# Kernel tuning notes

Hardware: AMD Instinct MI355X
Metric: run time of the kernel (lower is better)

The kernel has to match this reference:

```python
import jax, jax.numpy as jnp
import numpy as np

H = 1024
IN = 512
B = 32
E_H = 0.5
Z_MIN = 0.001
Z_MAX = 0.1
DT = 1.0


def setup_inputs() -> dict:
    key = jax.random.key(0)
    ks = jax.random.split(key, 10)
    s = 1.0 / np.sqrt(H)
    uni = lambda k, shape: jax.random.uniform(k, shape, jnp.float32, -s, s)
    return {
        "x": jax.random.normal(ks[0], (IN, B), jnp.float32),
        "h": jax.random.uniform(ks[1], (B, H), jnp.float32),      # hidden state [B,H]
        "X": jnp.ones((B, H, H), jnp.float32),                     # resources
        "U": jnp.full((B, H, H), 0.9, jnp.float32),                # utilization (init 0.9)
        "c_x": uni(ks[2], (H, H)),
        "c_u": uni(ks[3], (H, H)),
        "c_U": uni(ks[4], (H, H)),
        "c_h": uni(ks[5], (H, 1)),
        "w": uni(ks[6], (H, H)),
        "p": uni(ks[7], (H, IN)),
        "b": uni(ks[8], (H, 1)),
    }


def reference(x, h, X, U, c_x, c_u, c_U, c_h, w, p, b):
    sig = jax.nn.sigmoid
    hb = h[:, :, None]                                  # h[b,j] broadcast over k -> [B,H,1]
    # resource (X) update: z_x + (1-z_x)*X - dt*U*X*h
    z_x = Z_MIN + (Z_MAX - Z_MIN) * sig(c_x)            # [H,H]
    X_new = z_x + (1.0 - z_x) * X - DT * U * (X * hb)   # [B,H,H]
    # utilization (U) update, clamped to [Ucap (detached), 1]
    z_u = Z_MIN + (Z_MAX - Z_MIN) * sig(c_u)            # [H,H]
    Ucap = 0.9 * sig(c_U)                               # [H,H]
    U_new = Ucap * z_u + (1.0 - z_u) * U + DT * Ucap * ((1.0 - U) * hb)
    U_new = jnp.clip(U_new, jax.lax.stop_gradient(Ucap), 1.0)
    # hidden update with dynamic weights W = w * U * X (per batch)
    z_h = E_H * sig(c_h)                                # [H,1]
    W = w * U_new * X_new                               # [B,H,H]
    rec = jnp.einsum("bjk,bk->jb", W, h)               # [H,B]
    pre = rec + p @ x + b                               # [H,B]
    h_newT = (1.0 - z_h) * h.T + z_h * sig(pre)         # [H,B]
    return h_newT.T                                     # [B,H]
```

## Files before the change

### kernel.cpp

```cpp
#include <hip/hip_runtime.h>

#define HH 1024
#define INW 512
#define BB 32
#define BG 4
#define Z_MIN_C 0.001f
#define Z_RANGE_C 0.099f
#define E_H_C 0.5f

typedef float v4f __attribute__((ext_vector_type(4)));

__device__ __forceinline__ float sigmoidf_(float v) {
    return 1.0f / (1.0f + __expf(-v));
}

__global__ __launch_bounds__(256, 4) void stp_fused(
    const float* __restrict__ x,
    const float* __restrict__ h,
    const float* __restrict__ X,
    const float* __restrict__ U,
    const float* __restrict__ c_x,
    const float* __restrict__ c_u,
    const float* __restrict__ c_U,
    const float* __restrict__ c_h,
    const float* __restrict__ w,
    const float* __restrict__ p,
    const float* __restrict__ bias,
    float* __restrict__ out)
{
    const int j = blockIdx.x & (HH - 1);
    const int g = blockIdx.x >> 10;
    const int t = threadIdx.x;
    const int lane = t & 63;
    const int wave = t >> 6;
    const int k0 = t * 4;

    __shared__ float px_part[64][BG];
    __shared__ float rec_part[BG][4];

    v4f Xb[BG], Ub[BG], hkb[BG];
    float hjb[BG];
    #pragma unroll
    for (int i = 0; i < BG; ++i) {
        const int b = g * BG + i;
        const int rb = (b * HH + j) * HH + k0;
        Xb[i] = __builtin_nontemporal_load((const v4f*)(X + rb));
        Ub[i] = __builtin_nontemporal_load((const v4f*)(U + rb));
        hkb[i] = *(const v4f*)(h + b * HH + k0);
        hjb[i] = h[b * HH + j];
    }

    {
        const int b_id = t & 3;
        const int seg = t >> 2;
        const int b = g * BG + b_id;
        float acc = 0.0f;
        const float* prow = p + j * INW + seg * 8;
        const float* xcol = x + (seg * 8) * BB + b;
        #pragma unroll
        for (int i = 0; i < 8; ++i)
            acc = fmaf(prow[i], xcol[i * BB], acc);
        px_part[seg][b_id] = acc;
    }

    v4f cx4 = *(const v4f*)(c_x + j * HH + k0);
    v4f cu4 = *(const v4f*)(c_u + j * HH + k0);
    v4f cC4 = *(const v4f*)(c_U + j * HH + k0);
    v4f wv4 = *(const v4f*)(w + j * HH + k0);

    float zx[4], ozx[4], Acoef[4], ozu[4], Ucap[4], wr[4];
    #pragma unroll
    for (int c = 0; c < 4; ++c) {
        float zxx = Z_MIN_C + Z_RANGE_C * sigmoidf_(cx4[c]);
        float zuu = Z_MIN_C + Z_RANGE_C * sigmoidf_(cu4[c]);
        float ucc = 0.9f * sigmoidf_(cC4[c]);
        zx[c] = zxx;
        ozx[c] = 1.0f - zxx;
        ozu[c] = 1.0f - zuu;
        Ucap[c] = ucc;
        Acoef[c] = ucc * zuu;
        wr[c] = wv4[c];
    }

    float s[BG];
    #pragma unroll
    for (int i = 0; i < BG; ++i) {
        const float hjv = hjb[i];
        float ss = 0.0f;
        #pragma unroll
        for (int c = 0; c < 4; ++c) {
            float Xn = fmaf(ozx[c], Xb[i][c], zx[c]);
            Xn = fmaf(-Ub[i][c], Xb[i][c] * hjv, Xn);
            float Un = fmaf(ozu[c], Ub[i][c], Acoef[c]);
            Un = fmaf(Ucap[c] * hjv, 1.0f - Ub[i][c], Un);
            Un = fminf(fmaxf(Un, Ucap[c]), 1.0f);
            ss = fmaf(wr[c] * hkb[i][c], Un * Xn, ss);
        }
        s[i] = ss;
    }

    #pragma unroll
    for (int i = 0; i < BG; ++i) {
        float v = s[i];
        #pragma unroll
        for (int off = 32; off > 0; off >>= 1)
            v += __shfl_xor(v, off);
        if (lane == 0) rec_part[i][wave] = v;
    }
    __syncthreads();

    if (t < BG) {
        const int b = g * BG + t;
        float rec = rec_part[t][0] + rec_part[t][1] + rec_part[t][2] + rec_part[t][3];
        float px = 0.0f;
        #pragma unroll
        for (int sgi = 0; sgi < 64; ++sgi) px += px_part[sgi][t];
        float pre = rec + px + bias[j];
        float zh = E_H_C * sigmoidf_(c_h[j]);
        float hv = h[b * HH + j];
        out[b * HH + j] = (1.0f - zh) * hv + zh * sigmoidf_(pre);
    }
}

extern "C" void kernel_launch(void* const* d_in, const int* in_sizes, int n_in,
                              void* d_out, int out_size, void* d_ws, size_t ws_size,
                              hipStream_t stream) {
    const float* x   = (const float*)d_in[0];
    const float* h   = (const float*)d_in[1];
    const float* X   = (const float*)d_in[2];
    const float* U   = (const float*)d_in[3];
    const float* c_x = (const float*)d_in[4];
    const float* c_u = (const float*)d_in[5];
    const float* c_U = (const float*)d_in[6];
    const float* c_h = (const float*)d_in[7];
    const float* w   = (const float*)d_in[8];
    const float* p   = (const float*)d_in[9];
    const float* b   = (const float*)d_in[10];
    float* out = (float*)d_out;

    stp_fused<<<HH * 8, 256, 0, stream>>>(x, h, X, U, c_x, c_u, c_U, c_h, w, p, b, out);
}
```

Baseline: 299.8 us.

## Hoist p@x input projection into a separate precompute kernel

Moves the p@x + bias computation out of the fused kernel into a small prepass kernel that writes pre-activations to workspace. Before, each of the 8 batch-group blocks per row recomputed its own slice of p@x, so every p row was read 8 times, and the blocks needed shared-memory partials and a 64-term serial reduction. The main kernel now just reads one precomputed value per output. In exchange it adds a second launch and a workspace round trip. The prepass also reads x with a strided access pattern.

```diff
diff --git a/kernel.cpp b/kernel.cpp
--- a/kernel.cpp
+++ b/kernel.cpp
@@ -14,8 +14,30 @@
     return 1.0f / (1.0f + __expf(-v));
 }
 
+__global__ __launch_bounds__(256) void px_kernel(
+    const float* __restrict__ x,
+    const float* __restrict__ p,
+    const float* __restrict__ bias,
+    float* __restrict__ pre0)
+{
+    const int wv = threadIdx.x >> 6;
+    const int lane = threadIdx.x & 63;
+    const int j = blockIdx.x * 4 + wv;
+    const int b = lane & 31;
+    const int half = lane >> 5;
+
+    const float* pr = p + j * INW + half * 256;
+    const float* xc = x + (half * 256) * BB + b;
+    float acc = 0.0f;
+    #pragma unroll 8
+    for (int i = 0; i < 256; ++i)
+        acc = fmaf(pr[i], xc[i * BB], acc);
+    acc += __shfl_xor(acc, 32);
+    if (lane < 32)
+        pre0[lane * HH + j] = acc + bias[j];
+}
+
 __global__ __launch_bounds__(256, 4) void stp_fused(
-    const float* __restrict__ x,
     const float* __restrict__ h,
     const float* __restrict__ X,
     const float* __restrict__ U,
@@ -24,8 +46,7 @@
     const float* __restrict__ c_U,
     const float* __restrict__ c_h,
     const float* __restrict__ w,
-    const float* __restrict__ p,
-    const float* __restrict__ bias,
+    const float* __restrict__ pre0,
     float* __restrict__ out)
 {
     const int j = blockIdx.x & (HH - 1);
@@ -35,7 +56,6 @@
     const int wave = t >> 6;
     const int k0 = t * 4;
 
-    __shared__ float px_part[64][BG];
     __shared__ float rec_part[BG][4];
 
     v4f Xb[BG], Ub[BG], hkb[BG];
@@ -48,19 +68,6 @@
         Ub[i] = __builtin_nontemporal_load((const v4f*)(U + rb));
         hkb[i] = *(const v4f*)(h + b * HH + k0);
         hjb[i] = h[b * HH + j];
-    }
-
-    {
-        const int b_id = t & 3;
-        const int seg = t >> 2;
-        const int b = g * BG + b_id;
-        float acc = 0.0f;
-        const float* prow = p + j * INW + seg * 8;
-        const float* xcol = x + (seg * 8) * BB + b;
-        #pragma unroll
-        for (int i = 0; i < 8; ++i)
-            acc = fmaf(prow[i], xcol[i * BB], acc);
-        px_part[seg][b_id] = acc;
     }
 
     v4f cx4 = *(const v4f*)(c_x + j * HH + k0);
@@ -112,10 +119,7 @@
     if (t < BG) {
         const int b = g * BG + t;
         float rec = rec_part[t][0] + rec_part[t][1] + rec_part[t][2] + rec_part[t][3];
-        float px = 0.0f;
-        #pragma unroll
-        for (int sgi = 0; sgi < 64; ++sgi) px += px_part[sgi][t];
-        float pre = rec + px + bias[j];
+        float pre = pre0[b * HH + j] + rec;
         float zh = E_H_C * sigmoidf_(c_h[j]);
         float hv = h[b * HH + j];
         out[b * HH + j] = (1.0f - zh) * hv + zh * sigmoidf_(pre);
@@ -137,6 +141,8 @@
     const float* p   = (const float*)d_in[9];
     const float* b   = (const float*)d_in[10];
     float* out = (float*)d_out;
+    float* pre0 = (float*)d_ws;
 
-    stp_fused<<<HH * 8, 256, 0, stream>>>(x, h, X, U, c_x, c_u, c_U, c_h, w, p, b, out);
+    px_kernel<<<HH / 4, 256, 0, stream>>>(x, p, b, pre0);
+    stp_fused<<<HH * 8, 256, 0, stream>>>(h, X, U, c_x, c_u, c_U, c_h, w, pre0, out);
 }
```

Result: no change. 297.9 us (-0.6%).
